# Optimization experiments

Hardware: AMD Instinct MI355X
Metric: run time of the kernel (lower is better)

## Reference

```python
import jax, jax.numpy as jnp
import numpy as np

# Static model configuration (matches init_kwargs)
Hh, Ww = 48, 48
L = Hh * Ww            # 2304 flattened lattice sites
NH, HD = 8, 32         # heads, head_dim
D = NH * HD            # d_model = 256
MLP = 1024
NL = 4                 # num transformer blocks
RADIUS = 2             # local attention window radius
MAXD = 7               # relative position clipping
NB = 2 * MAXD + 1      # bias buckets per axis = 15
EPS = 1e-6
B = 4


def _coords():
    ys = jnp.arange(Hh)
    xs = jnp.arange(Ww)
    yy, xx = jnp.meshgrid(ys, xs, indexing='ij')
    return jnp.stack([yy, xx], axis=-1).reshape(L, 2)  # (L,2) int


def _local_mask():
    c = _coords()
    dy = jnp.abs(c[:, None, 0] - c[None, :, 0])
    dx = jnp.abs(c[:, None, 1] - c[None, :, 1])
    dy = jnp.minimum(dy, Hh - dy)  # periodic (torus)
    dx = jnp.minimum(dx, Ww - dx)
    allowed = (dy <= RADIUS) & (dx <= RADIUS)
    return jnp.where(allowed, 0.0, -1e9).astype(jnp.float32)  # (L,L)


def _rel_bias(rel_emb):
    c = _coords()
    dy = c[:, None, 0] - c[None, :, 0]
    dx = c[:, None, 1] - c[None, :, 1]
    # shortest signed periodic differences
    dy = (dy + Hh // 2) % Hh - Hh // 2
    dx = (dx + Ww // 2) % Ww - Ww // 2
    dyb = (jnp.clip(dy, -MAXD, MAXD) + MAXD).astype(jnp.int32)
    dxb = (jnp.clip(dx, -MAXD, MAXD) + MAXD).astype(jnp.int32)
    return rel_emb[:, dyb, dxb]  # (NH, L, L)


def _ln(x, s, b):
    mu = jnp.mean(x, axis=-1, keepdims=True)
    var = jnp.var(x, axis=-1, keepdims=True)
    return (x - mu) * jax.lax.rsqrt(var + EPS) * s + b


def setup_inputs() -> dict:
    key = jax.random.key(0)
    ks = jax.random.split(key, 16)
    sc = 0.05
    inp = {
        'x': jax.random.randint(ks[0], (B, Hh, Ww), 0, 2, dtype=jnp.int32),
        'Win': jax.random.normal(ks[1], (3, D), jnp.float32) * sc,
        'b_in': jnp.zeros((D,), jnp.float32),
        'lnA_s': jnp.ones((NL, D), jnp.float32),
        'lnA_b': jnp.zeros((NL, D), jnp.float32),
        'Wq': jax.random.normal(ks[2], (NL, D, NH, HD), jnp.float32) * sc,
        'bq': jnp.zeros((NL, NH, HD), jnp.float32),
        'Wk': jax.random.normal(ks[3], (NL, D, NH, HD), jnp.float32) * sc,
        'bk': jnp.zeros((NL, NH, HD), jnp.float32),
        'Wv': jax.random.normal(ks[4], (NL, D, NH, HD), jnp.float32) * sc,
        'bv': jnp.zeros((NL, NH, HD), jnp.float32),
        'Wo': jax.random.normal(ks[5], (NL, NH, HD, D), jnp.float32) * sc,
        'bo': jnp.zeros((NL, D), jnp.float32),
        'lnB_s': jnp.ones((NL, D), jnp.float32),
        'lnB_b': jnp.zeros((NL, D), jnp.float32),
        'W1': jax.random.normal(ks[6], (NL, D, MLP), jnp.float32) * sc,
        'b1': jnp.zeros((NL, MLP), jnp.float32),
        'W2': jax.random.normal(ks[7], (NL, MLP, D), jnp.float32) * sc,
        'b2': jnp.zeros((NL, D), jnp.float32),
        'rel_emb': jax.random.normal(ks[8], (NH, NB, NB), jnp.float32) * 0.02,
        'lnF_s': jnp.ones((D,), jnp.float32),
        'lnF_b': jnp.zeros((D,), jnp.float32),
        'Wout': jax.random.normal(ks[9], (D, 1), jnp.float32) * sc,
        'bout': jnp.zeros((1,), jnp.float32),
    }
    return inp


def reference(x, Win, b_in, lnA_s, lnA_b, Wq, bq, Wk, bk, Wv, bv, Wo, bo,
              lnB_s, lnB_b, W1, b1, W2, b2, rel_emb, lnF_s, lnF_b, Wout, bout):
    xf = x.astype(jnp.float32)[..., None]                     # (B,H,W,1)
    ys = jnp.arange(Hh, dtype=jnp.float32) / max(Hh - 1, 1)
    xs = jnp.arange(Ww, dtype=jnp.float32) / max(Ww - 1, 1)
    yy, xx = jnp.meshgrid(ys, xs, indexing='ij')
    coords = jnp.broadcast_to(jnp.stack([yy, xx], -1), (x.shape[0], Hh, Ww, 2))
    feats = jnp.concatenate([xf, coords], -1).reshape(x.shape[0], L, 3)

    h = feats @ Win + b_in                                    # (B,L,D)

    # combined additive attention bias: local periodic mask + learned 2D rel-pos bias
    cb = _local_mask()[None, None] + _rel_bias(rel_emb)[None]  # (1,NH,L,L)
    scale = 1.0 / np.sqrt(HD).astype(np.float32)

    for i in range(NL):
        y = _ln(h, lnA_s[i], lnA_b[i])
        q = jnp.einsum('bld,dhe->blhe', y, Wq[i]) + bq[i]
        k = jnp.einsum('bld,dhe->blhe', y, Wk[i]) + bk[i]
        v = jnp.einsum('bld,dhe->blhe', y, Wv[i]) + bv[i]
        scores = jnp.einsum('bqhe,bkhe->bhqk', q, k) * scale + cb
        p = jax.nn.softmax(scores, axis=-1)
        att = jnp.einsum('bhqk,bkhe->bqhe', p, v)
        y = jnp.einsum('bqhe,hed->bqd', att, Wo[i]) + bo[i]
        h = h + y
        y = _ln(h, lnB_s[i], lnB_b[i])
        y = jax.nn.gelu(y @ W1[i] + b1[i]) @ W2[i] + b2[i]
        h = h + y

    h = _ln(h, lnF_s, lnF_b)
    logits = (h @ Wout + bout)[..., 0].reshape(x.shape[0], Hh, Ww)
    return logits
```

## Files before the change

kernel.cpp:

```cpp
#include <hip/hip_runtime.h>
#include <hip/hip_bf16.h>
#include <math.h>

#define NT_   9216
#define D_    256
#define NH_   8
#define HD_   32
#define L_    2304
#define HH_   48
#define WW_   48
#define MLP_  1024
#define NL_   4

typedef __attribute__((ext_vector_type(8))) short bf16x8;
typedef __attribute__((ext_vector_type(4))) float f32x4;

__device__ __forceinline__ float gelu_tanh(float x) {
    const float c0 = 0.7978845608028654f;
    const float c1 = 0.044715f;
    float u = c0 * (x + c1 * x * x * x);
    return 0.5f * x * (1.0f + tanhf(u));
}

__device__ __forceinline__ void gload16(const void* gsrc, void* ldst) {
    __builtin_amdgcn_global_load_lds(
        (const __attribute__((address_space(1))) void*)gsrc,
        (__attribute__((address_space(3))) void*)ldst, 16, 0, 0);
}

__global__ void tcvt_kernel(const float* __restrict__ in, __hip_bfloat16* __restrict__ out,
                            int K, int N, int inLayerStride, int outLayerStride) {
    __shared__ float t[32][33];
    int l = blockIdx.z;
    int n0 = blockIdx.x * 32, k0 = blockIdx.y * 32;
    int tx = threadIdx.x, ty = threadIdx.y;
    const float* src = in + (size_t)l * inLayerStride;
    #pragma unroll
    for (int r = 0; r < 32; r += 8)
        t[ty + r][tx] = src[(size_t)(k0 + ty + r) * N + n0 + tx];
    __syncthreads();
    __hip_bfloat16* dst = out + (size_t)l * outLayerStride;
    #pragma unroll
    for (int r = 0; r < 32; r += 8)
        dst[(size_t)(n0 + ty + r) * K + k0 + tx] = __float2bfloat16(t[tx][ty + r]);
}

__global__ void bcat_kernel(const float* __restrict__ bq, const float* __restrict__ bk,
                            const float* __restrict__ bv, float* __restrict__ bqkv) {
    int l = blockIdx.x, n = threadIdx.x;
    float v = (n < 256) ? bq[l * 256 + n] : (n < 512 ? bk[l * 256 + n - 256] : bv[l * 256 + n - 512]);
    bqkv[l * 768 + n] = v;
}

__global__ void embed_kernel(const int* __restrict__ x, const float* __restrict__ Win,
                             const float* __restrict__ b_in, float* __restrict__ h) {
    int t = blockIdx.x, d = threadIdx.x;
    int l = t % L_;
    int yy = l / WW_, xx = l % WW_;
    float xv = (float)x[t];
    float yn = yy * (1.0f / 47.0f);
    float xn = xx * (1.0f / 47.0f);
    h[t * D_ + d] = xv * Win[d] + yn * Win[D_ + d] + xn * Win[2 * D_ + d] + b_in[d];
}

__global__ void ln_kernel(const float* __restrict__ h, const float* __restrict__ s,
                          const float* __restrict__ bb, __hip_bfloat16* __restrict__ y) {
    int t = blockIdx.x, d = threadIdx.x;
    float v = h[t * D_ + d];
    float a = v, b2 = v * v;
    #pragma unroll
    for (int off = 32; off; off >>= 1) {
        a  += __shfl_xor(a,  off);
        b2 += __shfl_xor(b2, off);
    }
    __shared__ float red[8];
    int wave = threadIdx.x >> 6;
    if ((threadIdx.x & 63) == 0) { red[wave] = a; red[4 + wave] = b2; }
    __syncthreads();
    float sum   = red[0] + red[1] + red[2] + red[3];
    float sumsq = red[4] + red[5] + red[6] + red[7];
    float mu  = sum * (1.0f / D_);
    float var = sumsq * (1.0f / D_) - mu * mu;
    float rs  = rsqrtf(var + 1e-6f);
    y[t * D_ + d] = __float2bfloat16((v - mu) * rs * s[d] + bb[d]);
}

__global__ void attn_kernel(const float* __restrict__ qkv, const float* __restrict__ rel_emb,
                            __hip_bfloat16* __restrict__ att) {
    int t = blockIdx.x;
    int hh = threadIdx.x >> 5;
    int e  = threadIdx.x & 31;
    int b  = t / L_;
    int l  = t - b * L_;
    int yy = l / WW_, xx = l - yy * WW_;

    float qv = qkv[(size_t)t * 768 + hh * HD_ + e];
    const float scale = 0.17677669529663687f;

    float scores[25];
    int   nidx[25];
    #pragma unroll
    for (int oy = -2; oy <= 2; ++oy) {
        #pragma unroll
        for (int ox = -2; ox <= 2; ++ox) {
            int j = (oy + 2) * 5 + (ox + 2);
            int ny = yy + oy; ny += (ny < 0) ? HH_ : 0; ny -= (ny >= HH_) ? HH_ : 0;
            int nx = xx + ox; nx += (nx < 0) ? WW_ : 0; nx -= (nx >= WW_) ? WW_ : 0;
            int nt = b * L_ + ny * WW_ + nx;
            nidx[j] = nt;
            float kv = qkv[(size_t)nt * 768 + 256 + hh * HD_ + e];
            float dot = qv * kv;
            #pragma unroll
            for (int off = 16; off; off >>= 1) dot += __shfl_xor(dot, off, 32);
            float bias = rel_emb[hh * 225 + (7 - oy) * 15 + (7 - ox)];
            scores[j] = dot * scale + bias;
        }
    }
    float m = scores[0];
    #pragma unroll
    for (int j = 1; j < 25; ++j) m = fmaxf(m, scores[j]);
    float sum = 0.0f;
    #pragma unroll
    for (int j = 0; j < 25; ++j) { scores[j] = expf(scores[j] - m); sum += scores[j]; }
    float inv = 1.0f / sum;
    float acc = 0.0f;
    #pragma unroll
    for (int j = 0; j < 25; ++j) acc += scores[j] * qkv[(size_t)nidx[j] * 768 + 512 + hh * HD_ + e];
    att[t * D_ + hh * HD_ + e] = __float2bfloat16(acc * inv);
}

template<int EPI>
__global__ __launch_bounds__(256, 2)
void mgemm(const __hip_bfloat16* __restrict__ A, const __hip_bfloat16* __restrict__ BT,
           const float* __restrict__ bias, const float* res,
           float* Cf, __hip_bfloat16* Cb, int M, int N, int K) {
    __shared__ __hip_bfloat16 As[128 * 32];
    __shared__ __hip_bfloat16 Bs[128 * 32];
    const int bm = blockIdx.y * 128, bn = blockIdx.x * 128;
    const int tid = threadIdx.x, lane = tid & 63, wv = tid >> 6;
    const int wm = (wv >> 1) * 64, wn = (wv & 1) * 64;

    const __hip_bfloat16* aSrc = A + (size_t)(bm + 16 * wv + (lane >> 2)) * K + (lane & 3) * 8;
    const __hip_bfloat16* bSrc = BT + (size_t)(bn + 16 * wv + (lane >> 2)) * K + (lane & 3) * 8;
    __hip_bfloat16* aDst0 = As + wv * 512;
    __hip_bfloat16* aDst1 = As + (wv + 4) * 512;
    __hip_bfloat16* bDst0 = Bs + wv * 512;
    __hip_bfloat16* bDst1 = Bs + (wv + 4) * 512;
    const size_t rowJump = (size_t)64 * K;

    f32x4 acc[4][4];
    #pragma unroll
    for (int i = 0; i < 4; ++i)
        #pragma unroll
        for (int j = 0; j < 4; ++j)
            acc[i][j] = (f32x4){0.f, 0.f, 0.f, 0.f};

    const int rsel = (lane & 15);
    const int ko   = (lane >> 4) * 8;

    for (int k0 = 0; k0 < K; k0 += 32) {
        gload16(aSrc,            aDst0);
        gload16(aSrc + rowJump,  aDst1);
        gload16(bSrc,            bDst0);
        gload16(bSrc + rowJump,  bDst1);
        __syncthreads();

        bf16x8 af[4], bfr[4];
        #pragma unroll
        for (int f = 0; f < 4; ++f) {
            af[f]  = *(const bf16x8*)(As + (wm + f * 16 + rsel) * 32 + ko);
            bfr[f] = *(const bf16x8*)(Bs + (wn + f * 16 + rsel) * 32 + ko);
        }
        #pragma unroll
        for (int i = 0; i < 4; ++i)
            #pragma unroll
            for (int j = 0; j < 4; ++j)
                acc[i][j] = __builtin_amdgcn_mfma_f32_16x16x32_bf16(af[i], bfr[j], acc[i][j], 0, 0, 0);
        __syncthreads();
        aSrc += 32; bSrc += 32;
    }

    #pragma unroll
    for (int i = 0; i < 4; ++i) {
        #pragma unroll
        for (int r = 0; r < 4; ++r) {
            int rr = bm + wm + i * 16 + (lane >> 4) * 4 + r;
            #pragma unroll
            for (int j = 0; j < 4; ++j) {
                int cc = bn + wn + j * 16 + rsel;
                float v = acc[i][j][r] + bias[cc];
                if (EPI == 2) {
                    Cb[(size_t)rr * N + cc] = __float2bfloat16(gelu_tanh(v));
                } else {
                    if (EPI == 1) v += res[(size_t)rr * N + cc];
                    Cf[(size_t)rr * N + cc] = v;
                }
            }
        }
    }
}

__global__ void final_kernel(const float* __restrict__ h, const float* __restrict__ s,
                             const float* __restrict__ bb, const float* __restrict__ Wout,
                             const float* __restrict__ bout, float* __restrict__ out) {
    int t = blockIdx.x, d = threadIdx.x;
    float v = h[t * D_ + d];
    float a = v, b2 = v * v;
    #pragma unroll
    for (int off = 32; off; off >>= 1) {
        a  += __shfl_xor(a,  off);
        b2 += __shfl_xor(b2, off);
    }
    __shared__ float red[8];
    __shared__ float red2[4];
    int wave = threadIdx.x >> 6;
    if ((threadIdx.x & 63) == 0) { red[wave] = a; red[4 + wave] = b2; }
    __syncthreads();
    float sum   = red[0] + red[1] + red[2] + red[3];
    float sumsq = red[4] + red[5] + red[6] + red[7];
    float mu  = sum * (1.0f / D_);
    float var = sumsq * (1.0f / D_) - mu * mu;
    float rs  = rsqrtf(var + 1e-6f);
    float yv  = (v - mu) * rs * s[d] + bb[d];
    float p   = yv * Wout[d];
    #pragma unroll
    for (int off = 32; off; off >>= 1) p += __shfl_xor(p, off);
    if ((threadIdx.x & 63) == 0) red2[wave] = p;
    __syncthreads();
    if (threadIdx.x == 0)
        out[t] = red2[0] + red2[1] + red2[2] + red2[3] + bout[0];
}

extern "C" void kernel_launch(void* const* d_in, const int* in_sizes, int n_in,
                              void* d_out, int out_size, void* d_ws, size_t ws_size,
                              hipStream_t stream) {
    const int*   x       = (const int*)  d_in[0];
    const float* Win     = (const float*)d_in[1];
    const float* b_in    = (const float*)d_in[2];
    const float* lnA_s   = (const float*)d_in[3];
    const float* lnA_b   = (const float*)d_in[4];
    const float* Wq      = (const float*)d_in[5];
    const float* bq      = (const float*)d_in[6];
    const float* Wk      = (const float*)d_in[7];
    const float* bk      = (const float*)d_in[8];
    const float* Wv      = (const float*)d_in[9];
    const float* bv      = (const float*)d_in[10];
    const float* Wo      = (const float*)d_in[11];
    const float* bo      = (const float*)d_in[12];
    const float* lnB_s   = (const float*)d_in[13];
    const float* lnB_b   = (const float*)d_in[14];
    const float* W1      = (const float*)d_in[15];
    const float* b1      = (const float*)d_in[16];
    const float* W2      = (const float*)d_in[17];
    const float* b2      = (const float*)d_in[18];
    const float* rel_emb = (const float*)d_in[19];
    const float* lnF_s   = (const float*)d_in[20];
    const float* lnF_b   = (const float*)d_in[21];
    const float* Wout    = (const float*)d_in[22];
    const float* bout    = (const float*)d_in[23];
    float* out = (float*)d_out;

    float* ws = (float*)d_ws;
    float*          h      = ws;
    __hip_bfloat16* y      = (__hip_bfloat16*)(ws + 2359296);
    float*          qkv    = ws + 3538944;
    __hip_bfloat16* att    = (__hip_bfloat16*)(ws + 10616832);
    __hip_bfloat16* tbuf   = (__hip_bfloat16*)qkv;
    __hip_bfloat16* WqkvT  = (__hip_bfloat16*)(ws + 11796480);
    __hip_bfloat16* WoT    = WqkvT + 4 * 768 * 256;
    __hip_bfloat16* W1T    = WoT   + 4 * 256 * 256;
    __hip_bfloat16* W2T    = W1T   + 4 * 1024 * 256;
    float*          bqkv   = (float*)(W2T + 4 * 256 * 1024);

    dim3 blk(256);
    dim3 tb(32, 8);

    tcvt_kernel<<<dim3(8, 8, 4),  tb, 0, stream>>>(Wq, WqkvT,              256, 256,  65536, 196608);
    tcvt_kernel<<<dim3(8, 8, 4),  tb, 0, stream>>>(Wk, WqkvT + 256 * 256,  256, 256,  65536, 196608);
    tcvt_kernel<<<dim3(8, 8, 4),  tb, 0, stream>>>(Wv, WqkvT + 512 * 256,  256, 256,  65536, 196608);
    tcvt_kernel<<<dim3(8, 8, 4),  tb, 0, stream>>>(Wo, WoT,                256, 256,  65536, 65536);
    tcvt_kernel<<<dim3(32, 8, 4), tb, 0, stream>>>(W1, W1T,                256, 1024, 262144, 262144);
    tcvt_kernel<<<dim3(8, 32, 4), tb, 0, stream>>>(W2, W2T,                1024, 256, 262144, 262144);
    bcat_kernel<<<4, 768, 0, stream>>>(bq, bk, bv, bqkv);

    embed_kernel<<<NT_, blk, 0, stream>>>(x, Win, b_in, h);

    for (int l = 0; l < NL_; ++l) {
        const __hip_bfloat16* wqkv = WqkvT + (size_t)l * 768 * 256;
        const __hip_bfloat16* wo   = WoT   + (size_t)l * 256 * 256;
        const __hip_bfloat16* w1   = W1T   + (size_t)l * 1024 * 256;
        const __hip_bfloat16* w2   = W2T   + (size_t)l * 256 * 1024;

        ln_kernel<<<NT_, blk, 0, stream>>>(h, lnA_s + l * D_, lnA_b + l * D_, y);

        mgemm<0><<<dim3(6, 72), blk, 0, stream>>>(y, wqkv, bqkv + l * 768, nullptr,
                                                  qkv, nullptr, NT_, 768, 256);
        attn_kernel<<<NT_, blk, 0, stream>>>(qkv, rel_emb, att);
        mgemm<1><<<dim3(2, 72), blk, 0, stream>>>(att, wo, bo + l * D_, h,
                                                  h, nullptr, NT_, 256, 256);

        ln_kernel<<<NT_, blk, 0, stream>>>(h, lnB_s + l * D_, lnB_b + l * D_, y);

        mgemm<2><<<dim3(8, 72), blk, 0, stream>>>(y, w1, b1 + l * MLP_, nullptr,
                                                  nullptr, tbuf, NT_, 1024, 256);
        mgemm<1><<<dim3(2, 72), blk, 0, stream>>>(tbuf, w2, b2 + l * D_, h,
                                                  h, nullptr, NT_, 256, 1024);
    }

    final_kernel<<<NT_, blk, 0, stream>>>(h, lnF_s, lnF_b, Wout, bout, out);
}
```

Measured before the change: 760.3 us.

## Use one wave per token in layernorm and lane-per-neighbor attention

LayerNorm now gives each token a single 64-lane wave with float4 loads and ushort4 bf16 stores. This removes the shared-memory reduction and the __syncthreads, and a block covers four tokens. The local attention kernel now assigns one lane per neighbor (25 of 32 lanes) to compute a full 32-dim dot product with vector loads. Softmax then runs as wave shuffle reductions, and the V accumulation broadcasts weights and row indices by shuffle. This replaces 25 serial shuffle reductions per thread, at the cost of 7 idle lanes and using __expf.

Result: no change. 747.9 us (-1.6%).

```diff
diff --git a/kernel.cpp b/kernel.cpp
--- a/kernel.cpp
+++ b/kernel.cpp
@@ -28,6 +28,11 @@
         (__attribute__((address_space(3))) void*)ldst, 16, 0, 0);
 }
 
+__device__ __forceinline__ unsigned short f2bf(float f) {
+    __hip_bfloat16 h = __float2bfloat16(f);
+    return *(unsigned short*)&h;
+}
+
 __global__ void tcvt_kernel(const float* __restrict__ in, __hip_bfloat16* __restrict__ out,
                             int K, int N, int inLayerStride, int outLayerStride) {
     __shared__ float t[32][33];
@@ -65,68 +70,77 @@
 
 __global__ void ln_kernel(const float* __restrict__ h, const float* __restrict__ s,
                           const float* __restrict__ bb, __hip_bfloat16* __restrict__ y) {
-    int t = blockIdx.x, d = threadIdx.x;
-    float v = h[t * D_ + d];
-    float a = v, b2 = v * v;
+    int wid = threadIdx.x >> 6, lane = threadIdx.x & 63;
+    int t = (blockIdx.x << 2) + wid;
+    float4 v = *(const float4*)(h + (size_t)t * D_ + lane * 4);
+    float sum = v.x + v.y + v.z + v.w;
+    float sq  = v.x * v.x + v.y * v.y + v.z * v.z + v.w * v.w;
     #pragma unroll
     for (int off = 32; off; off >>= 1) {
-        a  += __shfl_xor(a,  off);
-        b2 += __shfl_xor(b2, off);
-    }
-    __shared__ float red[8];
-    int wave = threadIdx.x >> 6;
-    if ((threadIdx.x & 63) == 0) { red[wave] = a; red[4 + wave] = b2; }
-    __syncthreads();
-    float sum   = red[0] + red[1] + red[2] + red[3];
-    float sumsq = red[4] + red[5] + red[6] + red[7];
+        sum += __shfl_xor(sum, off);
+        sq  += __shfl_xor(sq,  off);
+    }
     float mu  = sum * (1.0f / D_);
-    float var = sumsq * (1.0f / D_) - mu * mu;
+    float var = sq * (1.0f / D_) - mu * mu;
     float rs  = rsqrtf(var + 1e-6f);
-    y[t * D_ + d] = __float2bfloat16((v - mu) * rs * s[d] + bb[d]);
+    float4 s4 = *(const float4*)(s  + lane * 4);
+    float4 b4 = *(const float4*)(bb + lane * 4);
+    ushort4 o;
+    o.x = f2bf((v.x - mu) * rs * s4.x + b4.x);
+    o.y = f2bf((v.y - mu) * rs * s4.y + b4.y);
+    o.z = f2bf((v.z - mu) * rs * s4.z + b4.z);
+    o.w = f2bf((v.w - mu) * rs * s4.w + b4.w);
+    *(ushort4*)(y + (size_t)t * D_ + lane * 4) = o;
 }
 
 __global__ void attn_kernel(const float* __restrict__ qkv, const float* __restrict__ rel_emb,
                             __hip_bfloat16* __restrict__ att) {
-    int t = blockIdx.x;
-    int hh = threadIdx.x >> 5;
-    int e  = threadIdx.x & 31;
-    int b  = t / L_;
-    int l  = t - b * L_;
-    int yy = l / WW_, xx = l - yy * WW_;
-
-    float qv = qkv[(size_t)t * 768 + hh * HD_ + e];
-    const float scale = 0.17677669529663687f;
-
-    float scores[25];
-    int   nidx[25];
-    #pragma unroll
-    for (int oy = -2; oy <= 2; ++oy) {
-        #pragma unroll
-        for (int ox = -2; ox <= 2; ++ox) {
-            int j = (oy + 2) * 5 + (ox + 2);
-            int ny = yy + oy; ny += (ny < 0) ? HH_ : 0; ny -= (ny >= HH_) ? HH_ : 0;
-            int nx = xx + ox; nx += (nx < 0) ? WW_ : 0; nx -= (nx >= WW_) ? WW_ : 0;
-            int nt = b * L_ + ny * WW_ + nx;
-            nidx[j] = nt;
-            float kv = qkv[(size_t)nt * 768 + 256 + hh * HD_ + e];
-            float dot = qv * kv;
-            #pragma unroll
-            for (int off = 16; off; off >>= 1) dot += __shfl_xor(dot, off, 32);
-            float bias = rel_emb[hh * 225 + (7 - oy) * 15 + (7 - ox)];
-            scores[j] = dot * scale + bias;
-        }
-    }
-    float m = scores[0];
-    #pragma unroll
-    for (int j = 1; j < 25; ++j) m = fmaxf(m, scores[j]);
-    float sum = 0.0f;
-    #pragma unroll
-    for (int j = 0; j < 25; ++j) { scores[j] = expf(scores[j] - m); sum += scores[j]; }
+    const int t  = blockIdx.x;
+    const int hh = threadIdx.x >> 5;
+    const int j  = threadIdx.x & 31;
+    const int b  = t / L_;
+    const int l  = t - b * L_;
+    const int yy = l / WW_, xx = l - yy * WW_;
+
+    int oy2 = j / 5, ox2 = j - oy2 * 5;
+    bool valid = (j < 25);
+    int ny = yy + oy2 - 2; ny += (ny < 0) ? HH_ : 0; ny -= (ny >= HH_) ? HH_ : 0;
+    int nx = xx + ox2 - 2; nx += (nx < 0) ? WW_ : 0; nx -= (nx >= WW_) ? WW_ : 0;
+    int rowidx = valid ? (b * L_ + ny * WW_ + nx) : t;
+
+    const float* qp = qkv + (size_t)t * 768 + hh * HD_;
+    float4 q4[8];
+    #pragma unroll
+    for (int d = 0; d < 8; ++d) q4[d] = ((const float4*)qp)[d];
+
+    const float* kp = qkv + (size_t)rowidx * 768 + 256 + hh * HD_;
+    float dot = 0.f;
+    #pragma unroll
+    for (int d = 0; d < 8; ++d) {
+        float4 k4 = ((const float4*)kp)[d];
+        dot += q4[d].x * k4.x + q4[d].y * k4.y + q4[d].z * k4.z + q4[d].w * k4.w;
+    }
+    float bias = rel_emb[hh * 225 + (9 - oy2) * 15 + (9 - ox2)];
+    float s = valid ? (dot * 0.17677669529663687f + bias) : -1e30f;
+
+    float m = s;
+    #pragma unroll
+    for (int off = 16; off; off >>= 1) m = fmaxf(m, __shfl_xor(m, off, 32));
+    float p = __expf(s - m);
+    float sum = p;
+    #pragma unroll
+    for (int off = 16; off; off >>= 1) sum += __shfl_xor(sum, off, 32);
     float inv = 1.0f / sum;
-    float acc = 0.0f;
-    #pragma unroll
-    for (int j = 0; j < 25; ++j) acc += scores[j] * qkv[(size_t)nidx[j] * 768 + 512 + hh * HD_ + e];
-    att[t * D_ + hh * HD_ + e] = __float2bfloat16(acc * inv);
+
+    const float* vbase = qkv + 512 + hh * HD_ + j;
+    float acc = 0.f;
+    #pragma unroll
+    for (int n = 0; n < 25; ++n) {
+        float pn = __shfl(p, n, 32);
+        int   rn = __shfl(rowidx, n, 32);
+        acc += pn * vbase[(size_t)rn * 768];
+    }
+    att[t * D_ + hh * HD_ + j] = __float2bfloat16(acc * inv);
 }
 
 template<int EPI>
@@ -291,7 +305,7 @@
         const __hip_bfloat16* w1   = W1T   + (size_t)l * 1024 * 256;
         const __hip_bfloat16* w2   = W2T   + (size_t)l * 256 * 1024;
 
-        ln_kernel<<<NT_, blk, 0, stream>>>(h, lnA_s + l * D_, lnA_b + l * D_, y);
+        ln_kernel<<<NT_ / 4, blk, 0, stream>>>(h, lnA_s + l * D_, lnA_b + l * D_, y);
 
         mgemm<0><<<dim3(6, 72), blk, 0, stream>>>(y, wqkv, bqkv + l * 768, nullptr,
                                                   qkv, nullptr, NT_, 768, 256);
@@ -299,7 +313,7 @@
         mgemm<1><<<dim3(2, 72), blk, 0, stream>>>(att, wo, bo + l * D_, h,
                                                   h, nullptr, NT_, 256, 256);
 
-        ln_kernel<<<NT_, blk, 0, stream>>>(h, lnB_s + l * D_, lnB_b + l * D_, y);
+        ln_kernel<<<NT_ / 4, blk, 0, stream>>>(h, lnB_s + l * D_, lnB_b + l * D_, y);
 
         mgemm<2><<<dim3(8, 72), blk, 0, stream>>>(y, w1, b1 + l * MLP_, nullptr,
                                                   nullptr, tbuf, NT_, 1024, 256);
```
